# Optimization experiments

Measured on AMD Instinct MI355X. Metric: run time of the kernel, lower is better.

## Reference

```python
import jax, jax.numpy as jnp
import numpy as np

VEC_DIM = 3          # Cl(3,0): 3 positive-signature basis vectors
BASIS_DIM = 1 << VEC_DIM  # 8 basis blades
BATCH, IN_F, OUT_F = 512, 512, 512


def cayley_table(n: int = VEC_DIM) -> np.ndarray:
    """Geometric-product tensor G[i, j, k] for Cl(n,0) with blades as bitmasks.
    e_a * e_b = sign(a,b) * e_{a XOR b}; Euclidean metric so e_i^2 = +1.
    Only 2^(2n) of the 2^(3n) entries are nonzero (highly sparse)."""
    dim = 1 << n
    G = np.zeros((dim, dim, dim), dtype=np.float32)
    for a in range(dim):
        for b in range(dim):
            # sign from counting transpositions to bring blade product to canonical order
            swaps, t = 0, a >> 1
            while t:
                swaps += bin(t & b).count("1")
                t >>= 1
            G[a, b, a ^ b] = -1.0 if (swaps & 1) else 1.0
    return G


def setup_inputs() -> dict:
    key = jax.random.key(0)
    kx, kw, kb = jax.random.split(key, 3)
    x = jax.random.normal(kx, (BATCH, IN_F, BASIS_DIM), dtype=jnp.float32)
    W = jax.random.normal(kw, (IN_F, OUT_F, BASIS_DIM), dtype=jnp.float32)
    b = jax.random.normal(kb, (OUT_F, BASIS_DIM), dtype=jnp.float32)
    G = jnp.asarray(cayley_table())  # exact Cl(3,0) geometric-product tensor
    return {"x": x, "W": W, "b": b, "G": G}


def reference(x, W, b, G):
    # out[b,o,k] = sum_{i,j,p} G[i,j,k] * x[b,p,i] * W[p,o,j]  (+ bias)
    out = jnp.einsum("ijk,bpi,poj->bok", G, x, W)
    return out + b
```

## Files before the change

kernel.cpp:

```cpp
#include <hip/hip_runtime.h>
#include <hip/hip_bf16.h>
#include <stdint.h>

typedef __attribute__((ext_vector_type(8))) short short8;
typedef __attribute__((ext_vector_type(4))) float floatx4;

__device__ __forceinline__ unsigned short bfu(float a) {
    return __builtin_bit_cast(unsigned short, __float2bfloat16(a));
}
__device__ __forceinline__ uint32_t pkbf(float a, float b) {
    return (uint32_t)bfu(a) | ((uint32_t)bfu(b) << 16);
}


__global__ __launch_bounds__(256) void pack_all(
    const float* __restrict__ x, const float* __restrict__ W,
    unsigned short* __restrict__ Abuf, unsigned short* __restrict__ BT)
{
    const int t = threadIdx.x;
    if (blockIdx.x < 512) {
        __shared__ unsigned short TX[4][1024];
        const int b = blockIdx.x;
        const float4* src = (const float4*)(x + ((size_t)b * 512 + 2 * t) * 8);
        float4 f[4] = {src[0], src[1], src[2], src[3]};
        #pragma unroll
        for (int pp = 0; pp < 2; ++pp) {
            const float a0 = f[2*pp].x, a1 = f[2*pp].y, a2 = f[2*pp].z, a3 = f[2*pp].w;
            const float a4 = f[2*pp+1].x, a5 = f[2*pp+1].y, a6 = f[2*pp+1].z, a7 = f[2*pp+1].w;
            const int c = 4 * t + 2 * pp;
            TX[0][c] = bfu(a0 + a4); TX[0][c+1] = bfu(a1 - a5);
            TX[1][c] = bfu(a3 + a7); TX[1][c+1] = bfu(a6 - a2);
            TX[2][c] = bfu(a1 + a5); TX[2][c+1] = bfu(a0 - a4);
            TX[3][c] = bfu(a6 + a2); TX[3][c+1] = bfu(a7 - a3);
        }
        __syncthreads();
        const int tr = t >> 6, off = (t & 63) * 16;
        uint4* dst = (uint4*)(Abuf + (size_t)(2*b + (tr >> 1)) * 2048 + (tr & 1) * 1024 + off);
        const uint4* s4 = (const uint4*)&TX[tr][off];
        dst[0] = s4[0]; dst[1] = s4[1];
    } else {
        const int wb = blockIdx.x - 512;
        const int pbase = (wb & 7) * 64;
        const int o0 = (wb >> 3) * 16;
        const int o = o0 + (t & 15);
        const int pc = t >> 4;
        float R[4][2][2], I[4][2][2];
        #pragma unroll
        for (int u = 0; u < 4; ++u) {
            const float4* src = (const float4*)(W + ((size_t)(pbase + pc * 4 + u) * 512 + o) * 8);
            float4 lo = src[0], hi = src[1];
            R[u][0][0] = lo.x + hi.x;  I[u][0][0] = lo.w + hi.w;
            R[u][0][1] = lo.y - hi.y;  I[u][0][1] = hi.z - lo.z;
            R[u][1][0] = lo.y + hi.y;  I[u][1][0] = hi.z + lo.z;
            R[u][1][1] = lo.x - hi.x;  I[u][1][1] = hi.w - lo.w;
        }
        const int kbase = 2 * pbase + pc * 8;
        #pragma unroll
        for (int part = 0; part < 2; ++part)
            #pragma unroll
            for (int pN = 0; pN < 2; ++pN)
                #pragma unroll
                for (int c = 0; c < 2; ++c) {
                    uint4 v; uint32_t* vv = (uint32_t*)&v;
                    #pragma unroll
                    for (int u = 0; u < 4; ++u) {
                        const float v0 = (part == 0) ? (pN ? I[u][0][c] : R[u][0][c])
                                                     : (pN ? R[u][0][c] : -I[u][0][c]);
                        const float v1 = (part == 0) ? (pN ? I[u][1][c] : R[u][1][c])
                                                     : (pN ? R[u][1][c] : -I[u][1][c]);
                        vv[u] = pkbf(v0, v1);
                    }
                    const int n = 4 * o + 2 * pN + c;
                    *(uint4*)&BT[(size_t)n * 2048 + part * 1024 + kbase] = v;
                }
    }
}

#define GLL(src, dstoff) \
    __builtin_amdgcn_global_load_lds((const __attribute__((address_space(1))) uint32_t*)(src), \
        (__attribute__((address_space(3))) uint32_t*)(smem + (dstoff)), 16, 0, 0)

__global__ __launch_bounds__(256, 2) void iso_gemm3(
    const unsigned short* __restrict__ AB,
    const unsigned short* __restrict__ BB,
    const float* __restrict__ bias,
    float*       __restrict__ out)
{
    __shared__ __align__(16) unsigned char smem[65536];
    const int t = threadIdx.x, lane = t & 63, wave = t >> 6;
    const int g = wave;
    const int l15 = lane & 15, q = lane >> 4;

    const int lin = blockIdx.y * 32 + blockIdx.x;
    const int xcd = lin & 7, sx = lin >> 3;
    const int tm = (xcd >> 2) * 8 + (sx & 7);
    const int tn = (xcd & 3) * 8 + (sx >> 3);
    const int m0 = tm * 64, v0 = tn * 64;

    const unsigned short* a_srcs[4]; int a_dst[4];
    const unsigned short* b_srcs[4]; int b_dst[4];
    #pragma unroll
    for (int i = 0; i < 4; ++i) {
        const int sid = (wave * 4 + i) * 64 + lane;
        const int row = sid >> 4, slot = sid & 15, chunk = slot ^ (row & 7);
        a_srcs[i] = AB + (size_t)(m0 + row) * 2048 + chunk * 8;
        a_dst[i] = (wave * 4 + i) * 1024;
        b_srcs[i] = BB + (size_t)(v0 + row) * 2048 + chunk * 8;
        b_dst[i] = 16384 + (wave * 4 + i) * 1024;
    }

    const int slot = (g * 4 + q) ^ (l15 & 7);
    const int a_off = l15 * 256 + slot * 16;
    const int b_off = 16384 + l15 * 256 + slot * 16;

    floatx4 acc[4][4] = {};

    #pragma unroll
    for (int i = 0; i < 4; ++i) { GLL(a_srcs[i], a_dst[i]); GLL(b_srcs[i], b_dst[i]); }

    for (int kt = 0; kt < 16; ++kt) {
        __syncthreads();
        const int cur = (kt & 1) * 32768;
        if (kt + 1 < 16) {
            const int nxt = ((kt + 1) & 1) * 32768;
            const int poff = (kt + 1) * 128;
            #pragma unroll
            for (int i = 0; i < 4; ++i) {
                GLL(a_srcs[i] + poff, nxt + a_dst[i]);
                GLL(b_srcs[i] + poff, nxt + b_dst[i]);
            }
        }
        short8 af[4], bf[4];
        #pragma unroll
        for (int fm = 0; fm < 4; ++fm)
            af[fm] = *(const short8*)&smem[cur + a_off + fm * 4096];
        #pragma unroll
        for (int fn = 0; fn < 4; ++fn)
            bf[fn] = *(const short8*)&smem[cur + b_off + fn * 4096];
        #pragma unroll
        for (int fm = 0; fm < 4; ++fm)
            #pragma unroll
            for (int fn = 0; fn < 4; ++fn)
                acc[fm][fn] = __builtin_amdgcn_mfma_f32_16x16x32_bf16(
                    af[fm], bf[fn], acc[fm][fn], 0, 0, 0);
    }

    __syncthreads();
    if (g > 0) {
        float* r = (float*)(smem + (g - 1) * 16384);
        #pragma unroll
        for (int f = 0; f < 16; ++f)
            *(floatx4*)&r[f * 256 + lane * 4] = acc[f >> 2][f & 3];
    }
    __syncthreads();
    if (g == 0) {
        #pragma unroll
        for (int gg = 1; gg < 4; ++gg) {
            const float* r = (const float*)(smem + (gg - 1) * 16384);
            #pragma unroll
            for (int f = 0; f < 16; ++f)
                acc[f >> 2][f & 3] += *(const floatx4*)&r[f * 256 + lane * 4];
        }
    }
    __syncthreads();
    float* Cf = (float*)smem;
    if (g == 0) {
        #pragma unroll
        for (int fm = 0; fm < 4; ++fm)
            #pragma unroll
            for (int fn = 0; fn < 4; ++fn)
                #pragma unroll
                for (int rr = 0; rr < 4; ++rr) {
                    const int row = fm * 16 + q * 4 + rr;
                    const int col = fn * 16 + l15;
                    Cf[row * 66 + col] = acc[fm][fn][rr];
                }
    }
    __syncthreads();
    const int b0 = m0 >> 1, o0 = v0 >> 2;
    #pragma unroll
    for (int rnd = 0; rnd < 2; ++rnd) {
        const int pi = rnd * 256 + t;
        const int o_l = pi & 15, b_l = pi >> 4;
        const float* r0 = &Cf[(2 * b_l) * 66 + 4 * o_l];
        const float* r1 = r0 + 66;
        const float Cr00 = r0[0], Cr01 = r0[1], Ci00 = r0[2], Ci01 = r0[3];
        const float Cr10 = r1[0], Cr11 = r1[1], Ci10 = r1[2], Ci11 = r1[3];
        const float a0 = 0.5f * (Cr00 + Cr11), a7 = 0.5f * (Ci00 + Ci11);
        const float a4 = 0.5f * (Cr00 - Cr11), a3 = 0.5f * (Ci00 - Ci11);
        const float a1 = 0.5f * (Cr01 + Cr10), a6 = 0.5f * (Ci01 + Ci10);
        const float a2 = 0.5f * (Ci10 - Ci01), a5 = 0.5f * (Cr10 - Cr01);
        const int o = o0 + o_l, b = b0 + b_l;
        const float* bp = bias + o * 8;
        float4 lo = {a0 + bp[0], a1 + bp[1], a2 + bp[2], a3 + bp[3]};
        float4 hi = {a4 + bp[4], a5 + bp[5], a6 + bp[6], a7 + bp[7]};
        float* op = out + ((size_t)b * 512 + o) * 8;
        *(float4*)op = lo;
        *(float4*)(op + 4) = hi;
    }
}

__device__ __align__(16) const uint32_t SGN[4][4] = {
    {0x00000000u, 0x80000000u, 0x80000000u, 0x80008000u},
    {0x80000000u, 0x00000000u, 0x00000000u, 0x00008000u},
    {0x80000000u, 0x80008000u, 0x00000000u, 0x80000000u},
    {0x00000000u, 0x00008000u, 0x80000000u, 0x00000000u},
};
__device__ __forceinline__ uint32_t swap16(uint32_t a) { return (a >> 16) | (a << 16); }
__device__ __forceinline__ uint4 xperm2(uint4 v, int kp) {
    const bool s1 = (kp & 1) != 0;
    uint32_t x1 = s1 ? v.y : v.x, y1 = s1 ? v.x : v.y, z1 = s1 ? v.w : v.z, w1 = s1 ? v.z : v.w;
    const bool s2 = (kp & 2) != 0;
    uint4 r; r.x = s2 ? z1 : x1; r.y = s2 ? w1 : y1; r.z = s2 ? x1 : z1; r.w = s2 ? y1 : w1;
    return r;
}
__global__ __launch_bounds__(512) void gp_linear_legacy(
    const float* __restrict__ xg_raw, const float* __restrict__ wg,
    const float* __restrict__ bias, float* __restrict__ out)
{
    __shared__ __align__(16) unsigned short As[128 * 64];
    __shared__ __align__(16) unsigned short Bs[8 * 64 * 8];
    const int t = threadIdx.x, lane = t & 63, wave = t >> 6;
    const int m0 = blockIdx.y * 128, n0 = blockIdx.x * 64;
    const int ap = t & 7, akp = (t >> 3) & 3, ab = t >> 5, ak0 = akp * 2;
    const uint4 mask = *(const uint4*)SGN[akp];
    const int wm = wave & 3, wnn = wave >> 2, l15 = lane & 15, q = lane >> 4;
    floatx4 acc[2][2] = {};
    const float4* xg = (const float4*)xg_raw;
    const int bg0 = m0 >> 3;
    float4 ax0, ax1, bw0, bw1;
    {
        const size_t aidx = ((size_t)(bg0 + ab) * 512 + ap) * 2;
        ax0 = xg[aidx]; ax1 = xg[aidx + 1];
        const float* gsrc = wg + (((size_t)wave * 512 + n0) << 3) + (lane << 3);
        bw0 = *(const float4*)gsrc; bw1 = *(const float4*)(gsrc + 4);
    }
    for (int kt = 0; kt < 64; ++kt) {
        __syncthreads();
        {
            uint4 v;
            v.x = pkbf(ax0.x, ax0.y); v.y = pkbf(ax0.z, ax0.w);
            v.z = pkbf(ax1.x, ax1.y); v.w = pkbf(ax1.z, ax1.w);
            uint4 pk = xperm2(v, akp), r0, p1, r1;
            r0.x = pk.x ^ mask.x; r0.y = pk.y ^ mask.y; r0.z = pk.z ^ mask.z; r0.w = pk.w ^ mask.w;
            p1.x = swap16(pk.x); p1.y = swap16(pk.y); p1.z = swap16(pk.z); p1.w = swap16(pk.w);
            r1.x = p1.x ^ mask.x; r1.y = p1.y ^ mask.y; r1.z = p1.z ^ mask.z; r1.w = p1.w ^ mask.w;
            const int row0 = ab * 8 + ak0;
            *(uint4*)&As[row0 * 64 + ((ap ^ ak0) << 3)] = r0;
            *(uint4*)&As[(row0 + 1) * 64 + ((ap ^ (ak0 + 1)) << 3)] = r1;
        }
        {
            uint4 b0;
            b0.x = pkbf(bw0.x, bw0.y); b0.y = pkbf(bw0.z, bw0.w);
            b0.z = pkbf(bw1.x, bw1.y); b0.w = pkbf(bw1.z, bw1.w);
            *(uint4*)&Bs[t << 3] = b0;
        }
        __syncthreads();
        if (kt + 1 < 64) {
            const int p0n = (kt + 1) * 8;
            const size_t aidx = ((size_t)(bg0 + ab) * 512 + p0n + ap) * 2;
            ax0 = xg[aidx]; ax1 = xg[aidx + 1];
            const float* gsrc = wg + (((size_t)(p0n + wave) * 512 + n0) << 3) + (lane << 3);
            bw0 = *(const float4*)gsrc; bw1 = *(const float4*)(gsrc + 4);
        }
        #pragma unroll
        for (int ks = 0; ks < 2; ++ks) {
            const int cb = ks * 4 + q;
            short8 a[2], bfr[2];
            #pragma unroll
            for (int fm = 0; fm < 2; ++fm) {
                const int row = wm * 32 + fm * 16 + l15;
                a[fm] = *(const short8*)&As[row * 64 + ((cb ^ (l15 & 7)) << 3)];
            }
            #pragma unroll
            for (int fn = 0; fn < 2; ++fn) {
                const int nl = wnn * 32 + fn * 16 + l15;
                bfr[fn] = *(const short8*)&Bs[((cb * 64) + nl) << 3];
            }
            #pragma unroll
            for (int fm = 0; fm < 2; ++fm)
                #pragma unroll
                for (int fn = 0; fn < 2; ++fn)
                    acc[fm][fn] = __builtin_amdgcn_mfma_f32_16x16x32_bf16(a[fm], bfr[fn], acc[fm][fn], 0, 0, 0);
        }
    }
    #pragma unroll
    for (int fm = 0; fm < 2; ++fm)
        #pragma unroll
        for (int fn = 0; fn < 2; ++fn) {
            const int n = n0 + wnn * 32 + fn * 16 + l15;
            #pragma unroll
            for (int r = 0; r < 4; ++r) {
                const int m = m0 + wm * 32 + fm * 16 + q * 4 + r;
                const int bi = m >> 3, k = m & 7;
                out[(size_t)bi * 4096 + n * 8 + k] = acc[fm][fn][r] + bias[n * 8 + k];
            }
        }
}

extern "C" void kernel_launch(void* const* d_in, const int* in_sizes, int n_in,
                              void* d_out, int out_size, void* d_ws, size_t ws_size,
                              hipStream_t stream) {
    const float* x  = (const float*)d_in[0];
    const float* W  = (const float*)d_in[1];
    const float* bb = (const float*)d_in[2];
    float* out = (float*)d_out;

    const size_t abytes = (size_t)1024 * 2048 * sizeof(unsigned short);
    const size_t bbytes = (size_t)2048 * 2048 * sizeof(unsigned short);
    if (ws_size >= abytes + bbytes) {
        unsigned short* Abuf = (unsigned short*)d_ws;
        unsigned short* Bbuf = (unsigned short*)((char*)d_ws + abytes);
        pack_all<<<768, 256, 0, stream>>>(x, W, Abuf, Bbuf);
        iso_gemm3<<<dim3(32, 16), 256, 0, stream>>>(Abuf, Bbuf, bb, out);
    } else {
        gp_linear_legacy<<<dim3(8, 32), dim3(512), 0, stream>>>(x, W, bb, out);
    }
}
```

Before: 89.62 us.

## Split GEMM K dimension across blocks and reduce partials in separate kernel

Replaces the single GEMM kernel, which split K across the four waves and reduced them in shared memory, with a split-K GEMM. Two blocks per 64x64 tile each cover half of K, and each wave owns a 32x32 sub-tile. The smaller shared footprint allows 4 blocks per CU and doubles the grid to 1024 blocks. Partial sums are written to a workspace buffer and combined, along with the Clifford recombination and bias, by a new reduce kernel. This trades the intra-block reduction and low occupancy for an extra launch and a global round trip of the partial results, and it needs a larger workspace.

```diff
diff --git a/kernel.cpp b/kernel.cpp
--- a/kernel.cpp
+++ b/kernel.cpp
@@ -80,112 +80,106 @@
     __builtin_amdgcn_global_load_lds((const __attribute__((address_space(1))) uint32_t*)(src), \
         (__attribute__((address_space(3))) uint32_t*)(smem + (dstoff)), 16, 0, 0)
 
-__global__ __launch_bounds__(256, 2) void iso_gemm3(
+__global__ __launch_bounds__(256, 4) void gemm_split(
     const unsigned short* __restrict__ AB,
     const unsigned short* __restrict__ BB,
-    const float* __restrict__ bias,
-    float*       __restrict__ out)
+    float* __restrict__ partial)
 {
-    __shared__ __align__(16) unsigned char smem[65536];
+    __shared__ __align__(16) unsigned char smem[32768];
     const int t = threadIdx.x, lane = t & 63, wave = t >> 6;
-    const int g = wave;
+    const int wm = wave & 1, wn = wave >> 1;
     const int l15 = lane & 15, q = lane >> 4;
 
     const int lin = blockIdx.y * 32 + blockIdx.x;
-    const int xcd = lin & 7, sx = lin >> 3;
-    const int tm = (xcd >> 2) * 8 + (sx & 7);
-    const int tn = (xcd & 3) * 8 + (sx >> 3);
+    const int xcd = lin & 7, s = lin >> 3;
+    const int ks = s & 1;
+    const int tn = (xcd & 3) * 8 + ((s >> 1) & 7);
+    const int tm = (xcd >> 2) * 8 + (s >> 4);
     const int m0 = tm * 64, v0 = tn * 64;
-
-    const unsigned short* a_srcs[4]; int a_dst[4];
-    const unsigned short* b_srcs[4]; int b_dst[4];
-    #pragma unroll
-    for (int i = 0; i < 4; ++i) {
-        const int sid = (wave * 4 + i) * 64 + lane;
-        const int row = sid >> 4, slot = sid & 15, chunk = slot ^ (row & 7);
-        a_srcs[i] = AB + (size_t)(m0 + row) * 2048 + chunk * 8;
-        a_dst[i] = (wave * 4 + i) * 1024;
-        b_srcs[i] = BB + (size_t)(v0 + row) * 2048 + chunk * 8;
-        b_dst[i] = 16384 + (wave * 4 + i) * 1024;
-    }
-
-    const int slot = (g * 4 + q) ^ (l15 & 7);
-    const int a_off = l15 * 256 + slot * 16;
-    const int b_off = 16384 + l15 * 256 + slot * 16;
-
-    floatx4 acc[4][4] = {};
-
-    #pragma unroll
-    for (int i = 0; i < 4; ++i) { GLL(a_srcs[i], a_dst[i]); GLL(b_srcs[i], b_dst[i]); }
+    const int kb0 = ks * 1024;
+
+    const unsigned short* a_srcs[2]; int a_dst[2];
+    const unsigned short* b_srcs[2]; int b_dst[2];
+    #pragma unroll
+    for (int i = 0; i < 2; ++i) {
+        const int sid = (wave * 2 + i) * 64 + lane;
+        const int row = sid >> 3, sp = sid & 7, ch = sp ^ (row & 7);
+        a_srcs[i] = AB + (size_t)(m0 + row) * 2048 + kb0 + ch * 8;
+        a_dst[i] = (wave * 2 + i) * 1024;
+        b_srcs[i] = BB + (size_t)(v0 + row) * 2048 + kb0 + ch * 8;
+        b_dst[i] = 8192 + (wave * 2 + i) * 1024;
+    }
+
+    floatx4 acc[2][2] = {};
+
+    #pragma unroll
+    for (int i = 0; i < 2; ++i) { GLL(a_srcs[i], a_dst[i]); GLL(b_srcs[i], b_dst[i]); }
 
     for (int kt = 0; kt < 16; ++kt) {
         __syncthreads();
-        const int cur = (kt & 1) * 32768;
+        const int cur = (kt & 1) * 16384;
         if (kt + 1 < 16) {
-            const int nxt = ((kt + 1) & 1) * 32768;
-            const int poff = (kt + 1) * 128;
-            #pragma unroll
-            for (int i = 0; i < 4; ++i) {
+            const int nxt = ((kt + 1) & 1) * 16384;
+            const int poff = (kt + 1) * 64;
+            #pragma unroll
+            for (int i = 0; i < 2; ++i) {
                 GLL(a_srcs[i] + poff, nxt + a_dst[i]);
                 GLL(b_srcs[i] + poff, nxt + b_dst[i]);
             }
         }
-        short8 af[4], bf[4];
-        #pragma unroll
-        for (int fm = 0; fm < 4; ++fm)
-            af[fm] = *(const short8*)&smem[cur + a_off + fm * 4096];
-        #pragma unroll
-        for (int fn = 0; fn < 4; ++fn)
-            bf[fn] = *(const short8*)&smem[cur + b_off + fn * 4096];
-        #pragma unroll
-        for (int fm = 0; fm < 4; ++fm)
-            #pragma unroll
-            for (int fn = 0; fn < 4; ++fn)
-                acc[fm][fn] = __builtin_amdgcn_mfma_f32_16x16x32_bf16(
-                    af[fm], bf[fn], acc[fm][fn], 0, 0, 0);
-    }
-
-    __syncthreads();
-    if (g > 0) {
-        float* r = (float*)(smem + (g - 1) * 16384);
-        #pragma unroll
-        for (int f = 0; f < 16; ++f)
-            *(floatx4*)&r[f * 256 + lane * 4] = acc[f >> 2][f & 3];
-    }
-    __syncthreads();
-    if (g == 0) {
-        #pragma unroll
-        for (int gg = 1; gg < 4; ++gg) {
-            const float* r = (const float*)(smem + (gg - 1) * 16384);
-            #pragma unroll
-            for (int f = 0; f < 16; ++f)
-                acc[f >> 2][f & 3] += *(const floatx4*)&r[f * 256 + lane * 4];
-        }
-    }
-    __syncthreads();
-    float* Cf = (float*)smem;
-    if (g == 0) {
-        #pragma unroll
-        for (int fm = 0; fm < 4; ++fm)
-            #pragma unroll
-            for (int fn = 0; fn < 4; ++fn)
+        #pragma unroll
+        for (int ks2 = 0; ks2 < 2; ++ks2) {
+            const int slot = (ks2 * 4 + q) ^ (l15 & 7);
+            short8 af[2], bf[2];
+            #pragma unroll
+            for (int fm = 0; fm < 2; ++fm)
+                af[fm] = *(const short8*)&smem[cur + ((wm * 32 + fm * 16 + l15) * 8 + slot) * 16];
+            #pragma unroll
+            for (int fn = 0; fn < 2; ++fn)
+                bf[fn] = *(const short8*)&smem[cur + 8192 + ((wn * 32 + fn * 16 + l15) * 8 + slot) * 16];
+            #pragma unroll
+            for (int fm = 0; fm < 2; ++fm)
                 #pragma unroll
-                for (int rr = 0; rr < 4; ++rr) {
-                    const int row = fm * 16 + q * 4 + rr;
-                    const int col = fn * 16 + l15;
-                    Cf[row * 66 + col] = acc[fm][fn][rr];
-                }
-    }
-    __syncthreads();
-    const int b0 = m0 >> 1, o0 = v0 >> 2;
+                for (int fn = 0; fn < 2; ++fn)
+                    acc[fm][fn] = __builtin_amdgcn_mfma_f32_16x16x32_bf16(
+                        af[fm], bf[fn], acc[fm][fn], 0, 0, 0);
+        }
+    }
+
+    float* pt = partial + ((size_t)((tm * 32 + tn) * 2 + ks)) * 4096;
+    #pragma unroll
+    for (int fm = 0; fm < 2; ++fm)
+        #pragma unroll
+        for (int fn = 0; fn < 2; ++fn)
+            #pragma unroll
+            for (int rr = 0; rr < 4; ++rr)
+                pt[(wm * 32 + fm * 16 + q * 4 + rr) * 64 + wn * 32 + fn * 16 + l15]
+                    = acc[fm][fn][rr];
+}
+
+__global__ __launch_bounds__(256) void reduce_out(
+    const float* __restrict__ partial, const float* __restrict__ bias,
+    float* __restrict__ out)
+{
+    const int tile = blockIdx.x;
+    const int tm = tile >> 5, tn = tile & 31;
+    const float* p0 = partial + (size_t)(tile * 2 + 0) * 4096;
+    const float* p1 = partial + (size_t)(tile * 2 + 1) * 4096;
+    const int b0 = tm * 32, o0 = tn * 16;
+    const int t = threadIdx.x;
     #pragma unroll
     for (int rnd = 0; rnd < 2; ++rnd) {
         const int pi = rnd * 256 + t;
         const int o_l = pi & 15, b_l = pi >> 4;
-        const float* r0 = &Cf[(2 * b_l) * 66 + 4 * o_l];
-        const float* r1 = r0 + 66;
-        const float Cr00 = r0[0], Cr01 = r0[1], Ci00 = r0[2], Ci01 = r0[3];
-        const float Cr10 = r1[0], Cr11 = r1[1], Ci10 = r1[2], Ci11 = r1[3];
+        const int r0i = (2 * b_l) * 64 + 4 * o_l;
+        const float4 q00 = *(const float4*)&p0[r0i];
+        const float4 q01 = *(const float4*)&p0[r0i + 64];
+        const float4 q10 = *(const float4*)&p1[r0i];
+        const float4 q11 = *(const float4*)&p1[r0i + 64];
+        const float Cr00 = q00.x + q10.x, Cr01 = q00.y + q10.y;
+        const float Ci00 = q00.z + q10.z, Ci01 = q00.w + q10.w;
+        const float Cr10 = q01.x + q11.x, Cr11 = q01.y + q11.y;
+        const float Ci10 = q01.z + q11.z, Ci11 = q01.w + q11.w;
         const float a0 = 0.5f * (Cr00 + Cr11), a7 = 0.5f * (Ci00 + Ci11);
         const float a4 = 0.5f * (Cr00 - Cr11), a3 = 0.5f * (Ci00 - Ci11);
         const float a1 = 0.5f * (Cr01 + Cr10), a6 = 0.5f * (Ci01 + Ci10);
@@ -264,8 +258,8 @@
             bw0 = *(const float4*)gsrc; bw1 = *(const float4*)(gsrc + 4);
         }
         #pragma unroll
-        for (int ks = 0; ks < 2; ++ks) {
-            const int cb = ks * 4 + q;
+        for (int ksx = 0; ksx < 2; ++ksx) {
+            const int cb = ksx * 4 + q;
             short8 a[2], bfr[2];
             #pragma unroll
             for (int fm = 0; fm < 2; ++fm) {
@@ -308,11 +302,14 @@
 
     const size_t abytes = (size_t)1024 * 2048 * sizeof(unsigned short);
     const size_t bbytes = (size_t)2048 * 2048 * sizeof(unsigned short);
-    if (ws_size >= abytes + bbytes) {
+    const size_t pbytes = (size_t)512 * 2 * 4096 * sizeof(float);
+    if (ws_size >= abytes + bbytes + pbytes) {
         unsigned short* Abuf = (unsigned short*)d_ws;
         unsigned short* Bbuf = (unsigned short*)((char*)d_ws + abytes);
+        float* part = (float*)((char*)d_ws + abytes + bbytes);
         pack_all<<<768, 256, 0, stream>>>(x, W, Abuf, Bbuf);
-        iso_gemm3<<<dim3(32, 16), 256, 0, stream>>>(Abuf, Bbuf, bb, out);
+        gemm_split<<<dim3(32, 32), 256, 0, stream>>>(Abuf, Bbuf, part);
+        reduce_out<<<512, 256, 0, stream>>>(part, bb, out);
     } else {
         gp_linear_legacy<<<dim3(8, 32), dim3(512), 0, stream>>>(x, W, bb, out);
     }
```

Measured after the change: 92.02 us. 1.03x slower.
